# Kernel tuning notes

Hardware: AMD Instinct MI355X
Metric: run time of the kernel (lower is better)

Reference implementation:

```python
import jax, jax.numpy as jnp
import numpy as np

E, K, MULT = 8, 2, 4          # num_experts, top_k, ffn mult
CF = 1.25                     # capacity_factor


def setup_inputs() -> dict:
    key = jax.random.key(0)
    ks = jax.random.split(key, 8)
    B, T, C = 4, 2048, 1024
    H = C * MULT
    s = 0.02
    return {
        "x": jax.random.normal(ks[0], (B, T, C), jnp.float32),
        "rw": jax.random.normal(ks[1], (E, C), jnp.float32) * s,   # router weight [E,C]
        "rb": jnp.zeros((E,), jnp.float32),                        # router bias
        "w1": jax.random.normal(ks[2], (E, C, H), jnp.float32) * s,
        "b1": jnp.zeros((E, H), jnp.float32),
        "w2": jax.random.normal(ks[3], (E, H, C), jnp.float32) * s,
        "b2": jnp.zeros((E, C), jnp.float32),
    }


def reference(x, rw, rb, w1, b1, w2, b2):
    B, T, C = x.shape
    N = B * T
    cap = int(CF * N / E)                      # static capacity per expert
    xf = x.reshape(N, C)
    logits = xf @ rw.T + rb                    # [N,E]
    probs = jax.nn.softmax(logits, axis=-1)
    topk_probs, topk_idx = jax.lax.top_k(probs, K)      # [N,K]
    topk_probs = topk_probs / topk_probs.sum(-1, keepdims=True)

    # Flatten (token, choice) row-major == torch.where(mask) ordering
    flat_idx = topk_idx.reshape(-1)            # [N*K] expert id per slot
    flat_gate = topk_probs.reshape(-1)         # [N*K]
    onehot = jax.nn.one_hot(flat_idx, E, dtype=jnp.int32)          # [N*K,E]
    pos = (jnp.cumsum(onehot, axis=0) - 1)[jnp.arange(N * K), flat_idx]  # rank within expert
    keep = pos < cap                           # first-come-first-served capacity drop
    tok = jnp.arange(N * K) // K               # owning token of each slot

    # Dispatch into [E, cap] buffers; dropped slots go to a dump slot at the end
    buf = jnp.where(keep, flat_idx * cap + pos, E * cap)
    gate_buf = jnp.zeros(E * cap + 1, x.dtype).at[buf].add(flat_gate)[:E * cap]
    tok_buf = jnp.zeros(E * cap + 1, jnp.int32).at[buf].set(tok)[:E * cap]

    inp = xf[tok_buf].reshape(E, cap, C)       # gathered expert inputs
    h = jax.nn.gelu(jnp.einsum('eic,ech->eih', inp, w1) + b1[:, None, :], approximate=False)
    out = jnp.einsum('eih,ehc->eic', h, w2) + b2[:, None, :]
    out = out * gate_buf.reshape(E, cap, 1)    # empty slots have gate 0 -> zero contribution

    y = jnp.zeros((N, C), x.dtype).at[tok_buf].add(out.reshape(E * cap, C))

    # Aux load-balancing loss
    imp = probs.sum(0)
    imp = imp / imp.sum()
    load = jnp.minimum(onehot.sum(0).astype(x.dtype), cap)   # kept token counts
    load = load / load.sum()
    aux_loss = (imp * load).sum() * (E ** 2)
    return y.reshape(B, T, C), aux_loss
```

## Files before the change

### kernel.cpp

```cpp
#include <hip/hip_runtime.h>
#include <hip/hip_bf16.h>
#include <math.h>

#define NE    8
#define KTOP  2
#define CDIM  1024
#define HDIM  4096
#define NTOK  8192
#define CAPE  1280
#define NSLOT (NTOK * KTOP)

typedef __bf16 bf16x8 __attribute__((ext_vector_type(8)));
typedef __bf16 bf16x4 __attribute__((ext_vector_type(4)));
typedef __bf16 bf16x2 __attribute__((ext_vector_type(2)));
typedef float  f32x4  __attribute__((ext_vector_type(4)));

#define GAS __attribute__((address_space(1)))
#define LAS __attribute__((address_space(3)))

__global__ __launch_bounds__(256) void k_transpose_bf16(
    const float* __restrict__ src, __bf16* __restrict__ dst, int R, int Cc)
{
    __shared__ float tile[32][33];
    const int e  = blockIdx.z;
    const int cb = blockIdx.x * 32;
    const int rb = blockIdx.y * 32;
    const int t  = threadIdx.x;
    const int tx = t & 31, ty = t >> 5;
    const float* s = src + (size_t)e * R * Cc;
    __bf16*      d = dst + (size_t)e * R * Cc;
#pragma unroll
    for (int i = 0; i < 32; i += 8)
        tile[ty + i][tx] = s[(size_t)(rb + ty + i) * Cc + cb + tx];
    __syncthreads();
    const int op  = t & 15;
    const int oc0 = t >> 4;
#pragma unroll
    for (int j = 0; j < 2; ++j) {
        const int oc = oc0 + j * 16;
        bf16x2 v;
        v[0] = (__bf16)tile[op * 2][oc];
        v[1] = (__bf16)tile[op * 2 + 1][oc];
        *(bf16x2*)(d + (size_t)(cb + oc) * R + rb + op * 2) = v;
    }
}

__global__ __launch_bounds__(256) void k_router(
    const float* __restrict__ x, const float* __restrict__ rw,
    const float* __restrict__ rb, float* __restrict__ probs,
    float* __restrict__ gates, int* __restrict__ tidx)
{
    __shared__ float rws[NE * CDIM];
    const int tid = threadIdx.x;
    for (int i = tid; i < NE * CDIM / 4; i += 256)
        ((float4*)rws)[i] = ((const float4*)rw)[i];
    __syncthreads();

    const int wave = tid >> 6, lane = tid & 63;
    const int n = blockIdx.x * 4 + wave;
    const float* xr = x + (size_t)n * CDIM;

    float acc[NE];
#pragma unroll
    for (int e = 0; e < NE; ++e) acc[e] = 0.f;
    for (int j = 0; j < CDIM / 64; ++j) {
        const float xv = xr[j * 64 + lane];
#pragma unroll
        for (int e = 0; e < NE; ++e) acc[e] += xv * rws[e * CDIM + j * 64 + lane];
    }
#pragma unroll
    for (int off = 32; off > 0; off >>= 1) {
#pragma unroll
        for (int e = 0; e < NE; ++e) acc[e] += __shfl_down(acc[e], off);
    }
    if (lane == 0) {
        float mx = -1e30f;
#pragma unroll
        for (int e = 0; e < NE; ++e) { acc[e] += rb[e]; mx = fmaxf(mx, acc[e]); }
        float p[NE], s = 0.f;
#pragma unroll
        for (int e = 0; e < NE; ++e) { p[e] = expf(acc[e] - mx); s += p[e]; }
        const float inv = 1.f / s;
#pragma unroll
        for (int e = 0; e < NE; ++e) { p[e] *= inv; probs[(size_t)n * NE + e] = p[e]; }
        int   i1 = 0;  float v1 = p[0];
        int   i2 = -1; float v2 = -1.f;
#pragma unroll
        for (int e = 1; e < NE; ++e) {
            if (p[e] > v1)      { v2 = v1; i2 = i1; v1 = p[e]; i1 = e; }
            else if (p[e] > v2) { v2 = p[e]; i2 = e; }
        }
        const float gs = 1.f / (v1 + v2);
        gates[n * 2 + 0] = v1 * gs;  gates[n * 2 + 1] = v2 * gs;
        tidx[n * 2 + 0]  = i1;       tidx[n * 2 + 1]  = i2;
    }
}

__global__ __launch_bounds__(256) void k_scan(
    const int* __restrict__ tidx, const float* __restrict__ probs,
    int* __restrict__ slot, int* __restrict__ tok, float* __restrict__ d_aux)
{
    __shared__ int   lcnt[256][NE];
    __shared__ float ps[256][NE];
    const int t = threadIdx.x;

    for (int i = t; i < NE * CAPE; i += 256) tok[i] = 0;

    int c8[NE];
#pragma unroll
    for (int e = 0; e < NE; ++e) c8[e] = 0;
    const int per  = NSLOT / 256;
    const int base = t * per;
    for (int s = 0; s < per; ++s) c8[tidx[base + s]]++;
#pragma unroll
    for (int e = 0; e < NE; ++e) lcnt[t][e] = c8[e];

    float f8[NE];
#pragma unroll
    for (int e = 0; e < NE; ++e) f8[e] = 0.f;
    for (int n = t; n < NTOK; n += 256) {
        const float4 a = *(const float4*)(probs + (size_t)n * NE);
        const float4 b = *(const float4*)(probs + (size_t)n * NE + 4);
        f8[0] += a.x; f8[1] += a.y; f8[2] += a.z; f8[3] += a.w;
        f8[4] += b.x; f8[5] += b.y; f8[6] += b.z; f8[7] += b.w;
    }
#pragma unroll
    for (int e = 0; e < NE; ++e) ps[t][e] = f8[e];

    __syncthreads();

    int pre[NE], tot[NE];
#pragma unroll
    for (int e = 0; e < NE; ++e) { pre[e] = 0; tot[e] = 0; }
    for (int tt = 0; tt < 256; ++tt) {
#pragma unroll
        for (int e = 0; e < NE; ++e) {
            const int v = lcnt[tt][e];
            tot[e] += v;
            if (tt < t) pre[e] += v;
        }
    }
    for (int s = 0; s < per; ++s) {
        const int sg = base + s;
        const int e  = tidx[sg];
        const int p  = pre[e]++;
        if (p < CAPE) { slot[sg] = e * CAPE + p; tok[e * CAPE + p] = sg >> 1; }
        else          { slot[sg] = -1; }
    }
    if (t == 0) {
        float imp[NE], isum = 0.f, ld[NE], lsum = 0.f;
#pragma unroll
        for (int e = 0; e < NE; ++e) {
            float v = 0.f;
            for (int tt = 0; tt < 256; ++tt) v += ps[tt][e];
            imp[e] = v; isum += v;
        }
#pragma unroll
        for (int e = 0; e < NE; ++e) { ld[e] = fminf((float)tot[e], (float)CAPE); lsum += ld[e]; }
        float aux = 0.f;
#pragma unroll
        for (int e = 0; e < NE; ++e) aux += (imp[e] / isum) * (ld[e] / lsum);
        *d_aux = aux * (float)(NE * NE);
    }
}

__global__ __launch_bounds__(256) void k_gather(
    const float* __restrict__ x, const int* __restrict__ tok,
    __bf16* __restrict__ inp)
{
    const int row = blockIdx.x;
    const int t   = threadIdx.x;
    const int tk  = tok[row];
    const float4 v = ((const float4*)(x + (size_t)tk * CDIM))[t];
    bf16x4 o;
    o[0] = (__bf16)v.x; o[1] = (__bf16)v.y; o[2] = (__bf16)v.z; o[3] = (__bf16)v.w;
    *(bf16x4*)(inp + (size_t)row * CDIM + t * 4) = o;
}

#define MFMA_BF16 __builtin_amdgcn_mfma_f32_16x16x32_bf16
#define DSR(dst, addr, IMM) \
    asm volatile("ds_read_b128 %0, %1 offset:" #IMM : "=v"(dst) : "v"(addr))
#define WLG0()  asm volatile("s_waitcnt lgkmcnt(0)" ::: "memory")
#define WVM0()  asm volatile("s_waitcnt vmcnt(0)" ::: "memory")
#define SB0()   __builtin_amdgcn_sched_barrier(0)

#define CLUSTER20()                                                           \
    __builtin_amdgcn_s_setprio(1);                                            \
    _Pragma("unroll")                                                         \
    for (int m = 0; m < 5; ++m) {                                             \
        _Pragma("unroll")                                                     \
        for (int n = 0; n < 4; ++n)                                           \
            acc[m][n] = MFMA_BF16(fb[n], fa[m], acc[m][n], 0, 0, 0);          \
    }                                                                         \
    __builtin_amdgcn_s_setprio(0);

template <bool GELU>
__global__ __launch_bounds__(512, 2) void k_gemm8(
    const __bf16* __restrict__ Aall, const __bf16* __restrict__ Ball,
    const float* __restrict__ biasAll, __bf16* __restrict__ Call,
    int Ktot, int Ntot, int NBN, int mtPerE)
{
    __shared__ char lds[114688];

    const int NK  = Ktot >> 6;
    const int cpx = gridDim.x >> 3;
    const int id  = blockIdx.x;
    const int sid = (id & 7) * cpx + (id >> 3);
    const int bm  = sid / NBN, bn = sid % NBN;
    const int e   = bm / mtPerE;

    const size_t row0 = (size_t)bm * 320;
    const int    col0 = bn * 128;

    const int tid = threadIdx.x;
    const int w   = tid >> 6, l = tid & 63;
    const int wr  = w >> 1, wc = w & 1;
    const int lr  = l & 15, hi = l >> 4;

    const int srow = (w << 3) + (l >> 3);
    const int kf   = ((l & 7) ^ (l >> 3)) << 3;
    const __bf16* pA = Aall + (row0 + srow) * (size_t)Ktot + kf;
    const __bf16* pB = Ball + ((size_t)e * Ntot + col0 + srow) * (size_t)Ktot + kf;
    const size_t rstep = (size_t)64 * Ktot;
    const unsigned L0  = (unsigned)(size_t)(LAS char*)lds;
    const unsigned dA0 = L0 + w * 1024;
    const unsigned dB0 = L0 + 81920 + w * 1024;

    auto STAGE_ALL = [&](unsigned abufo, unsigned bbufo, int kt) {
        const __bf16* ga = pA + (size_t)kt * 64;
        const __bf16* gb = pB + (size_t)kt * 64;
#pragma unroll
        for (int h = 0; h < 5; ++h)
            __builtin_amdgcn_global_load_lds(
                (const GAS void*)(ga + h * rstep),
                (LAS void*)(size_t)(dA0 + abufo + h * 8192), 16, 0, 0);
#pragma unroll
        for (int h = 0; h < 2; ++h)
            __builtin_amdgcn_global_load_lds(
                (const GAS void*)(gb + h * rstep),
                (LAS void*)(size_t)(dB0 + bbufo + h * 8192), 16, 0, 0);
    };

    const unsigned swz = (l & 7) << 4;
    const unsigned kb0 = ((unsigned)(hi << 4)) ^ swz;
    const unsigned kb1 = ((unsigned)(64 + (hi << 4))) ^ swz;
    const unsigned AbaseR = L0 + (unsigned)(wr * 80 + lr) * 128;
    const unsigned BbaseR = L0 + 81920 + (unsigned)(wc * 64 + lr) * 128;

    STAGE_ALL(0, 0, 0);
    WVM0();
    __builtin_amdgcn_s_barrier();
    SB0();

    f32x4 acc[5][4] = {};
    bf16x8 fa[5], fb[4];

    unsigned ab = 0, bb = 0;
    for (int T = 0; T < NK; ++T) {
        const unsigned va0 = AbaseR + ab + kb0, va1 = AbaseR + ab + kb1;
        const unsigned vb0 = BbaseR + bb + kb0, vb1 = BbaseR + bb + kb1;

        DSR(fa[0], va0, 0);    DSR(fa[1], va0, 2048); DSR(fa[2], va0, 4096);
        DSR(fa[3], va0, 6144); DSR(fa[4], va0, 8192);
        DSR(fb[0], vb0, 0);    DSR(fb[1], vb0, 2048);
        DSR(fb[2], vb0, 4096); DSR(fb[3], vb0, 6144);
        if (T + 1 < NK) STAGE_ALL(ab ^ 40960u, bb ^ 16384u, T + 1);
        __builtin_amdgcn_s_barrier();
        WLG0(); SB0();
        CLUSTER20()
        __builtin_amdgcn_s_barrier();
        SB0();

        DSR(fa[0], va1, 0);    DSR(fa[1], va1, 2048); DSR(fa[2], va1, 4096);
        DSR(fa[3], va1, 6144); DSR(fa[4], va1, 8192);
        DSR(fb[0], vb1, 0);    DSR(fb[1], vb1, 2048);
        DSR(fb[2], vb1, 4096); DSR(fb[3], vb1, 6144);
        __builtin_amdgcn_s_barrier();
        WLG0(); SB0();
        CLUSTER20()
        WVM0();
        __builtin_amdgcn_s_barrier();
        SB0();

        ab ^= 40960u; bb ^= 16384u;
    }

    const size_t crow0 = row0 + (size_t)wr * 80;
    const int    ccol0 = col0 + wc * 64;
#pragma unroll
    for (int n = 0; n < 4; ++n) {
        float bbv[4] = {0.f, 0.f, 0.f, 0.f};
        if (GELU) {
            const float4 b4 = *(const float4*)(biasAll + (size_t)e * Ntot
                                               + ccol0 + n * 16 + hi * 4);
            bbv[0] = b4.x; bbv[1] = b4.y; bbv[2] = b4.z; bbv[3] = b4.w;
        }
#pragma unroll
        for (int m = 0; m < 5; ++m) {
            const f32x4 v = acc[m][n];
            bf16x4 o;
#pragma unroll
            for (int i = 0; i < 4; ++i) {
                float t = v[i];
                if (GELU) {
                    t += bbv[i];
                    const float u  = 0.7978845608028654f * (t + 0.044715f * t * t * t);
                    const float ex = __expf(2.f * u);
                    t = t * (1.f - 1.f / (ex + 1.f));
                }
                o[i] = (__bf16)t;
            }
            *(bf16x4*)(Call + (crow0 + m * 16 + lr) * (size_t)Ntot
                       + ccol0 + n * 16 + hi * 4) = o;
        }
    }
}

__global__ __launch_bounds__(256) void k_combine(
    const __bf16* __restrict__ outb, const int* __restrict__ slot,
    const float* __restrict__ gates, const int* __restrict__ tidx,
    const float* __restrict__ b2, float* __restrict__ y)
{
    const int n = blockIdx.x;
    const int t = threadIdx.x;
    const int c = t * 4;
    float r0 = 0.f, r1 = 0.f, r2 = 0.f, r3 = 0.f;
#pragma unroll
    for (int k = 0; k < KTOP; ++k) {
        const int s = slot[n * 2 + k];
        if (s < 0) continue;
        const float g = gates[n * 2 + k];
        const int   e = tidx[n * 2 + k];
        const bf16x4 v = *(const bf16x4*)(outb + (size_t)s * CDIM + c);
        const float4 bb = *(const float4*)(b2 + (size_t)e * CDIM + c);
        r0 += g * ((float)v[0] + bb.x);
        r1 += g * ((float)v[1] + bb.y);
        r2 += g * ((float)v[2] + bb.z);
        r3 += g * ((float)v[3] + bb.w);
    }
    float4 o = make_float4(r0, r1, r2, r3);
    *(float4*)(y + (size_t)n * CDIM + c) = o;
}

extern "C" void kernel_launch(void* const* d_in, const int* in_sizes, int n_in,
                              void* d_out, int out_size, void* d_ws, size_t ws_size,
                              hipStream_t stream)
{
    const float* x  = (const float*)d_in[0];
    const float* rw = (const float*)d_in[1];
    const float* rb = (const float*)d_in[2];
    const float* w1 = (const float*)d_in[3];
    const float* b1 = (const float*)d_in[4];
    const float* w2 = (const float*)d_in[5];
    const float* b2 = (const float*)d_in[6];
    float* y = (float*)d_out;

    char* ws = (char*)d_ws;
    size_t off = 0;
    auto alloc = [&](size_t bytes) -> void* {
        void* p = ws + off;
        off = (off + bytes + 255) & ~(size_t)255;
        return p;
    };
    __bf16* w1t  = (__bf16*)alloc((size_t)NE * CDIM * HDIM * 2);
    __bf16* w2t  = (__bf16*)alloc((size_t)NE * CDIM * HDIM * 2);
    __bf16* inp  = (__bf16*)alloc((size_t)NE * CAPE * CDIM * 2);
    __bf16* hbuf = (__bf16*)alloc((size_t)NE * CAPE * HDIM * 2);
    __bf16* outb = (__bf16*)alloc((size_t)NE * CAPE * CDIM * 2);
    float*  probs = (float*)alloc((size_t)NTOK * NE * 4);
    float*  gates = (float*)alloc((size_t)NTOK * 2 * 4);
    int*    tidx  = (int*)alloc((size_t)NTOK * 2 * 4);
    int*    slot  = (int*)alloc((size_t)NTOK * 2 * 4);
    int*    tok   = (int*)alloc((size_t)NE * CAPE * 4);

    k_transpose_bf16<<<dim3(HDIM / 32, CDIM / 32, NE), 256, 0, stream>>>(
        w1, w1t, CDIM, HDIM);
    k_transpose_bf16<<<dim3(CDIM / 32, HDIM / 32, NE), 256, 0, stream>>>(
        w2, w2t, HDIM, CDIM);

    k_router<<<NTOK / 4, 256, 0, stream>>>(x, rw, rb, probs, gates, tidx);

    k_scan<<<1, 256, 0, stream>>>(tidx, probs, slot, tok, y + (size_t)NTOK * CDIM);

    k_gather<<<NE * CAPE, 256, 0, stream>>>(x, tok, inp);

    k_gemm8<true><<<dim3((NTOK * KTOP * 10 / 16 / 320) * (HDIM / 128)), 512, 0, stream>>>(
        inp, w1t, b1, hbuf, CDIM, HDIM, HDIM / 128, 4);
    k_gemm8<false><<<dim3((NTOK * KTOP * 10 / 16 / 320) * (CDIM / 128)), 512, 0, stream>>>(
        hbuf, w2t, nullptr, outb, HDIM, CDIM, CDIM / 128, 4);

    k_combine<<<NTOK, 256, 0, stream>>>(outb, slot, gates, tidx, b2, y);
}
```

Baseline: 407.3 us.

## Rework expert GEMM into smaller-tile triple-buffered pipeline with higher occupancy

The expert GEMM moves from 320x128 tiles with K-step 64 and double buffering to 256x128 tiles with K-step 32 and a three-stage LDS ring. Each iteration issues the prefetch two steps ahead and waits with a partial vmcnt instead of draining all loads. LDS use drops to 72KB and launch bounds rise to 4 blocks per CU, aiming for more overlap of memory and MFMA work and better latency hiding. In exchange, each tile reuses loaded data less, the loop runs more iterations with more barriers, and the LDS layout loses the previous XOR swizzle, which risks bank conflicts.

```diff
diff --git a/kernel.cpp b/kernel.cpp
--- a/kernel.cpp
+++ b/kernel.cpp
@@ -178,38 +178,27 @@
 }
 
 #define MFMA_BF16 __builtin_amdgcn_mfma_f32_16x16x32_bf16
-#define DSR(dst, addr, IMM) \
+#define DSR_I(dst, addr, IMM) \
     asm volatile("ds_read_b128 %0, %1 offset:" #IMM : "=v"(dst) : "v"(addr))
-#define WLG0()  asm volatile("s_waitcnt lgkmcnt(0)" ::: "memory")
-#define WVM0()  asm volatile("s_waitcnt vmcnt(0)" ::: "memory")
-#define SB0()   __builtin_amdgcn_sched_barrier(0)
-
-#define CLUSTER20()                                                           \
-    __builtin_amdgcn_s_setprio(1);                                            \
-    _Pragma("unroll")                                                         \
-    for (int m = 0; m < 5; ++m) {                                             \
-        _Pragma("unroll")                                                     \
-        for (int n = 0; n < 4; ++n)                                           \
-            acc[m][n] = MFMA_BF16(fb[n], fa[m], acc[m][n], 0, 0, 0);          \
-    }                                                                         \
-    __builtin_amdgcn_s_setprio(0);
+#define DSR(dst, addr, IMM) DSR_I(dst, addr, IMM)
+#define SB0()  __builtin_amdgcn_sched_barrier(0)
 
 template <bool GELU>
-__global__ __launch_bounds__(512, 2) void k_gemm8(
+__global__ __launch_bounds__(512, 4) void k_gemmT(
     const __bf16* __restrict__ Aall, const __bf16* __restrict__ Ball,
     const float* __restrict__ biasAll, __bf16* __restrict__ Call,
     int Ktot, int Ntot, int NBN, int mtPerE)
 {
-    __shared__ char lds[114688];
-
-    const int NK  = Ktot >> 6;
+    __shared__ char lds[73728];
+
+    const int NK  = Ktot >> 5;
     const int cpx = gridDim.x >> 3;
     const int id  = blockIdx.x;
     const int sid = (id & 7) * cpx + (id >> 3);
     const int bm  = sid / NBN, bn = sid % NBN;
     const int e   = bm / mtPerE;
 
-    const size_t row0 = (size_t)bm * 320;
+    const size_t row0 = (size_t)bm * 256;
     const int    col0 = bn * 128;
 
     const int tid = threadIdx.x;
@@ -217,75 +206,63 @@
     const int wr  = w >> 1, wc = w & 1;
     const int lr  = l & 15, hi = l >> 4;
 
-    const int srow = (w << 3) + (l >> 3);
-    const int kf   = ((l & 7) ^ (l >> 3)) << 3;
-    const __bf16* pA = Aall + (row0 + srow) * (size_t)Ktot + kf;
-    const __bf16* pB = Ball + ((size_t)e * Ntot + col0 + srow) * (size_t)Ktot + kf;
-    const size_t rstep = (size_t)64 * Ktot;
-    const unsigned L0  = (unsigned)(size_t)(LAS char*)lds;
-    const unsigned dA0 = L0 + w * 1024;
-    const unsigned dB0 = L0 + 81920 + w * 1024;
-
-    auto STAGE_ALL = [&](unsigned abufo, unsigned bbufo, int kt) {
-        const __bf16* ga = pA + (size_t)kt * 64;
-        const __bf16* gb = pB + (size_t)kt * 64;
-#pragma unroll
-        for (int h = 0; h < 5; ++h)
-            __builtin_amdgcn_global_load_lds(
-                (const GAS void*)(ga + h * rstep),
-                (LAS void*)(size_t)(dA0 + abufo + h * 8192), 16, 0, 0);
-#pragma unroll
-        for (int h = 0; h < 2; ++h)
-            __builtin_amdgcn_global_load_lds(
-                (const GAS void*)(gb + h * rstep),
-                (LAS void*)(size_t)(dB0 + bbufo + h * 8192), 16, 0, 0);
+    const int srow = tid >> 2;
+    const int kc   = (tid & 3) * 8;
+    const __bf16* pA = Aall + (row0 + srow) * (size_t)Ktot + kc;
+    const __bf16* pB = Ball + ((size_t)e * Ntot + col0 + srow) * (size_t)Ktot + kc;
+    const size_t rstepA = (size_t)128 * Ktot;
+    const unsigned L0 = (unsigned)(size_t)(LAS char*)lds;
+    const unsigned dA = L0 + w * 1024;
+    const unsigned dB = L0 + 16384 + w * 1024;
+
+    auto STAGE = [&](unsigned bo, int kt) {
+        const __bf16* ga = pA + (size_t)kt * 32;
+        const __bf16* gb = pB + (size_t)kt * 32;
+        __builtin_amdgcn_global_load_lds((const GAS void*)ga,
+            (LAS void*)(size_t)(dA + bo), 16, 0, 0);
+        __builtin_amdgcn_global_load_lds((const GAS void*)(ga + rstepA),
+            (LAS void*)(size_t)(dA + bo + 8192), 16, 0, 0);
+        __builtin_amdgcn_global_load_lds((const GAS void*)gb,
+            (LAS void*)(size_t)(dB + bo), 16, 0, 0);
     };
 
-    const unsigned swz = (l & 7) << 4;
-    const unsigned kb0 = ((unsigned)(hi << 4)) ^ swz;
-    const unsigned kb1 = ((unsigned)(64 + (hi << 4))) ^ swz;
-    const unsigned AbaseR = L0 + (unsigned)(wr * 80 + lr) * 128;
-    const unsigned BbaseR = L0 + 81920 + (unsigned)(wc * 64 + lr) * 128;
-
-    STAGE_ALL(0, 0, 0);
-    WVM0();
-    __builtin_amdgcn_s_barrier();
-    SB0();
-
-    f32x4 acc[5][4] = {};
-    bf16x8 fa[5], fb[4];
-
-    unsigned ab = 0, bb = 0;
+    const unsigned foff  = (unsigned)(lr * 64 + hi * 16);
+    const unsigned vaB = L0 + (unsigned)(wr * 4096) + foff;
+    const unsigned vbB = L0 + 16384 + (unsigned)(wc * 4096) + foff;
+
+    STAGE(0, 0);
+    STAGE(24576, (NK > 1) ? 1 : 0);
+
+    f32x4 acc[4][4] = {};
+    bf16x8 fa[4], fb[4];
+
+    unsigned cur = 0, stg = 49152;
     for (int T = 0; T < NK; ++T) {
-        const unsigned va0 = AbaseR + ab + kb0, va1 = AbaseR + ab + kb1;
-        const unsigned vb0 = BbaseR + bb + kb0, vb1 = BbaseR + bb + kb1;
-
-        DSR(fa[0], va0, 0);    DSR(fa[1], va0, 2048); DSR(fa[2], va0, 4096);
-        DSR(fa[3], va0, 6144); DSR(fa[4], va0, 8192);
-        DSR(fb[0], vb0, 0);    DSR(fb[1], vb0, 2048);
-        DSR(fb[2], vb0, 4096); DSR(fb[3], vb0, 6144);
-        if (T + 1 < NK) STAGE_ALL(ab ^ 40960u, bb ^ 16384u, T + 1);
-        __builtin_amdgcn_s_barrier();
-        WLG0(); SB0();
-        CLUSTER20()
+        asm volatile("s_waitcnt vmcnt(3)" ::: "memory");
         __builtin_amdgcn_s_barrier();
         SB0();
-
-        DSR(fa[0], va1, 0);    DSR(fa[1], va1, 2048); DSR(fa[2], va1, 4096);
-        DSR(fa[3], va1, 6144); DSR(fa[4], va1, 8192);
-        DSR(fb[0], vb1, 0);    DSR(fb[1], vb1, 2048);
-        DSR(fb[2], vb1, 4096); DSR(fb[3], vb1, 6144);
-        __builtin_amdgcn_s_barrier();
-        WLG0(); SB0();
-        CLUSTER20()
-        WVM0();
-        __builtin_amdgcn_s_barrier();
+        const unsigned va = vaB + cur, vb = vbB + cur;
+        DSR(fa[0], va, 0); DSR(fa[1], va, 1024);
+        DSR(fa[2], va, 2048); DSR(fa[3], va, 3072);
+        DSR(fb[0], vb, 0); DSR(fb[1], vb, 1024);
+        DSR(fb[2], vb, 2048); DSR(fb[3], vb, 3072);
+        int kt = T + 2; if (kt > NK - 1) kt = NK - 1;
+        STAGE(stg, kt);
+        asm volatile("s_waitcnt lgkmcnt(0)" ::: "memory");
         SB0();
-
-        ab ^= 40960u; bb ^= 16384u;
-    }
-
-    const size_t crow0 = row0 + (size_t)wr * 80;
+        __builtin_amdgcn_s_setprio(1);
+#pragma unroll
+        for (int n = 0; n < 4; ++n)
+#pragma unroll
+            for (int m = 0; m < 4; ++m)
+                acc[m][n] = MFMA_BF16(fb[n], fa[m], acc[m][n], 0, 0, 0);
+        __builtin_amdgcn_s_setprio(0);
+        SB0();
+        cur = (cur == 49152u) ? 0u : cur + 24576u;
+        stg = (stg == 49152u) ? 0u : stg + 24576u;
+    }
+
+    const size_t crow0 = row0 + (size_t)wr * 64;
     const int    ccol0 = col0 + wc * 64;
 #pragma unroll
     for (int n = 0; n < 4; ++n) {
@@ -296,7 +273,7 @@
             bbv[0] = b4.x; bbv[1] = b4.y; bbv[2] = b4.z; bbv[3] = b4.w;
         }
 #pragma unroll
-        for (int m = 0; m < 5; ++m) {
+        for (int m = 0; m < 4; ++m) {
             const f32x4 v = acc[m][n];
             bf16x4 o;
 #pragma unroll
@@ -384,10 +361,10 @@
 
     k_gather<<<NE * CAPE, 256, 0, stream>>>(x, tok, inp);
 
-    k_gemm8<true><<<dim3((NTOK * KTOP * 10 / 16 / 320) * (HDIM / 128)), 512, 0, stream>>>(
-        inp, w1t, b1, hbuf, CDIM, HDIM, HDIM / 128, 4);
-    k_gemm8<false><<<dim3((NTOK * KTOP * 10 / 16 / 320) * (CDIM / 128)), 512, 0, stream>>>(
-        hbuf, w2t, nullptr, outb, HDIM, CDIM, CDIM / 128, 4);
+    k_gemmT<true><<<dim3((NE * CAPE / 256) * (HDIM / 128)), 512, 0, stream>>>(
+        inp, w1t, b1, hbuf, CDIM, HDIM, HDIM / 128, CAPE / 256);
+    k_gemmT<false><<<dim3((NE * CAPE / 256) * (CDIM / 128)), 512, 0, stream>>>(
+        hbuf, w2t, nullptr, outb, HDIM, CDIM, CDIM / 128, CAPE / 256);
 
     k_combine<<<NTOK, 256, 0, stream>>>(outb, slot, gates, tidx, b2, y);
 }
```

New measurement: 424.4 us. +4.2%, slower.
